# Kernel tuning notes

Measured on AMD Instinct MI355X. Metric: run time of the kernel, lower is better.

Reference implementation:

```python
import jax, jax.numpy as jnp
import numpy as np

B, N, N_IN, N_HID, N_OUT, T = 64, 64, 64, 256, 64, 4
E = N * (N - 1)  # 4032 directed edges, fully connected minus self-loops


def _incidence():
    # off-diagonal sender/receiver index pairs, NRI-style one-hot matrices
    send_idx, rec_idx = [], []
    for i in range(N):
        for j in range(N):
            if i != j:
                send_idx.append(i)
                rec_idx.append(j)
    eye = np.eye(N, dtype=np.float32)
    rel_send = eye[np.array(send_idx)]  # [E, N]
    rel_rec = eye[np.array(rec_idx)]    # [E, N]
    return jnp.asarray(rel_rec), jnp.asarray(rel_send)


def setup_inputs() -> dict:
    key = jax.random.key(0)
    ks = jax.random.split(key, 16)
    rel_rec, rel_send = _incidence()
    s1 = 1.0 / np.sqrt(2 * N_IN)
    s2 = 1.0 / np.sqrt(N_HID)
    s3 = 1.0 / np.sqrt(N_IN + N_OUT)
    return {
        "x": jax.random.normal(ks[0], (B, N, N_IN), jnp.float32),
        "rel_type": jax.random.uniform(ks[1], (B, E, T), jnp.float32),
        "rel_rec": rel_rec,
        "rel_send": rel_send,
        # per-edge-type message MLPs, stored as [T, in, out] (torch Linear transposed)
        "w1": jax.random.uniform(ks[2], (T, 2 * N_IN, N_HID), jnp.float32, -s1, s1),
        "b1": jax.random.uniform(ks[3], (T, N_HID), jnp.float32, -s1, s1),
        "w2": jax.random.uniform(ks[4], (T, N_HID, N_OUT), jnp.float32, -s2, s2),
        "b2": jax.random.uniform(ks[5], (T, N_OUT), jnp.float32, -s2, s2),
        "ow1": jax.random.uniform(ks[6], (N_IN + N_OUT, N_HID), jnp.float32, -s3, s3),
        "ob1": jax.random.uniform(ks[7], (N_HID,), jnp.float32, -s3, s3),
        "ow2": jax.random.uniform(ks[8], (N_HID, N_HID), jnp.float32, -s2, s2),
        "ob2": jax.random.uniform(ks[9], (N_HID,), jnp.float32, -s2, s2),
        "ow3": jax.random.uniform(ks[10], (N_HID, N_OUT), jnp.float32, -s2, s2),
        "ob3": jax.random.uniform(ks[11], (N_OUT,), jnp.float32, -s2, s2),
    }


def reference(x, rel_type, rel_rec, rel_send, w1, b1, w2, b2, ow1, ob1, ow2, ob2, ow3, ob3):
    # node2edge gather: [E,N] @ [B,N,F] -> [B,E,F]
    receivers = jnp.einsum('en,bnf->bef', rel_rec, x)
    senders = jnp.einsum('en,bnf->bef', rel_send, x)
    pre_msg = jnp.concatenate([senders, receivers], axis=-1)  # [B,E,2F]
    all_msgs = jnp.zeros((pre_msg.shape[0], pre_msg.shape[1], w2.shape[-1]), pre_msg.dtype)
    for i in range(w1.shape[0]):  # small fixed edge_types loop (structurally distinct weights)
        m = jax.nn.relu(pre_msg @ w1[i] + b1[i])           # [B,E,H]
        m = jax.nn.relu(m @ w2[i] + b2[i])                 # [B,E,O]
        all_msgs = all_msgs + m * rel_type[:, :, i:i + 1]  # weighted accumulate
    # edge2node scatter-aggregate: [N,E] @ [B,E,O] -> [B,N,O]
    agg_msgs = jnp.einsum('en,beo->bno', rel_rec, all_msgs)
    aug = jnp.concatenate([x, agg_msgs], axis=-1)          # [B,N,F+O]
    h = jax.nn.relu(aug @ ow1 + ob1)
    h = jax.nn.relu(h @ ow2 + ob2)
    return h @ ow3 + ob3                                   # [B,N,O]
```

## Files before the change

kernel.cpp:

```cpp
#include <hip/hip_runtime.h>

typedef unsigned short u16;
typedef __attribute__((ext_vector_type(8))) _Float16 f16x8;
typedef __attribute__((ext_vector_type(2))) _Float16 f16x2;
typedef __attribute__((ext_vector_type(4))) float f32x4;

#define DEV static __device__ __forceinline__

DEV float bf2f(u16 h){ unsigned u = ((unsigned)h) << 16; return __builtin_bit_cast(float, u); }
DEV u16 f2bf(float f){ unsigned u = __builtin_bit_cast(unsigned, f); u += 0x7FFFu + ((u >> 16) & 1u); return (u16)(u >> 16); }
DEV u16 f2h(float f){ _Float16 h = (_Float16)f; return __builtin_bit_cast(u16, h); }
DEV float h2f(u16 h){ return (float)__builtin_bit_cast(_Float16, h); }

DEV f32x4 mfma16(f16x8 a, f16x8 b, f32x4 c){
  return __builtin_amdgcn_mfma_f32_16x16x32_f16(a, b, c, 0, 0, 0);
}

DEV unsigned rap(unsigned a, unsigned b){
  f16x2 ha = __builtin_bit_cast(f16x2, a);
  f16x2 hb = __builtin_bit_cast(f16x2, b);
  f16x2 s = ha + hb;
  const _Float16 z = (_Float16)0;
  s.x = s.x > z ? s.x : z;
  s.y = s.y > z ? s.y : z;
  return __builtin_bit_cast(unsigned, s);
}

DEV f16x8 build_frag(uint4 s, uint4 r){
  uint4 o;
  o.x = rap(s.x, r.x); o.y = rap(s.y, r.y);
  o.z = rap(s.z, r.z); o.w = rap(s.w, r.w);
  return __builtin_bit_cast(f16x8, o);
}

#define OFF_W1T  256
#define OFF_W2T  262400
#define OFF_OW1T 393472
#define OFF_OW2T 459008
#define OFF_OW3T 590080
#define OFF_B1   622848
#define OFF_B2   624896
#define OFF_OB1  625408
#define OFF_OB2  625920
#define OFF_OB3  626432
#define OFF_XC   626688
#define OFF_RTC  1150976
#define OFF_S1   3215360
#define OFF_R1   11603968
#define OFF_AGG  19992576

__global__ void k_sniff(const u16* __restrict__ x, int* __restrict__ flag){
  int l = threadIdx.x;
  u16 u = x[2 * l];
  int e = (u >> 7) & 0xFF;
  int ok = (e >= 103 && e <= 143) ? 1 : 0;
  unsigned long long m = __ballot(ok);
  if(l == 0) *flag = (__builtin_popcountll(m) >= 40) ? 1 : 0;
}

DEV float ldin(const void* p, int i, int isbf){
  return isbf ? bf2f(((const u16*)p)[i]) : ((const float*)p)[i];
}

__global__ __launch_bounds__(256) void k_tr(const void* __restrict__ w1, const void* __restrict__ w2,
    const void* __restrict__ ow1, const void* __restrict__ ow2, const void* __restrict__ ow3,
    char* __restrict__ ws){
  const int isbf = *(const int*)ws;
  __shared__ float tile[32][33];
  int bid = blockIdx.x, tid = threadIdx.x;
  const void* src; u16* dst; int R, C, off, r0, c0;
  if(bid < 128){ int g = bid >> 5, tt = bid & 31;
    src = w1; dst = (u16*)(ws + OFF_W1T); R = 128; C = 256; off = g * 32768;
    r0 = (tt >> 3) << 5; c0 = (tt & 7) << 5;
  } else if(bid < 192){ int bb = bid - 128; int g = bb >> 4, tt = bb & 15;
    src = w2; dst = (u16*)(ws + OFF_W2T); R = 256; C = 64; off = g * 16384;
    r0 = (tt >> 1) << 5; c0 = (tt & 1) << 5;
  } else if(bid < 224){ int bb = bid - 192;
    src = ow1; dst = (u16*)(ws + OFF_OW1T); R = 128; C = 256; off = 0;
    r0 = (bb >> 3) << 5; c0 = (bb & 7) << 5;
  } else if(bid < 288){ int bb = bid - 224;
    src = ow2; dst = (u16*)(ws + OFF_OW2T); R = 256; C = 256; off = 0;
    r0 = (bb >> 3) << 5; c0 = (bb & 7) << 5;
  } else { int bb = bid - 288;
    src = ow3; dst = (u16*)(ws + OFF_OW3T); R = 256; C = 64; off = 0;
    r0 = (bb >> 1) << 5; c0 = (bb & 1) << 5;
  }
  int tx = tid & 31, ty = tid >> 5;
  #pragma unroll
  for(int p = 0; p < 4; ++p){
    int r = ty + p * 8;
    tile[r][tx] = ldin(src, off + (r0 + r) * C + c0 + tx, isbf);
  }
  __syncthreads();
  #pragma unroll
  for(int p = 0; p < 4; ++p){
    int c = ty + p * 8;
    dst[off + (c0 + c) * R + r0 + tx] = f2h(tile[tx][c]);
  }
}

__global__ __launch_bounds__(256) void k_cvt2(const void* __restrict__ x, const void* __restrict__ rt,
    const void* __restrict__ b1, const void* __restrict__ b2,
    const void* __restrict__ ob1, const void* __restrict__ ob2, const void* __restrict__ ob3,
    char* __restrict__ ws){
  const int isbf = *(const int*)ws;
  int n = blockIdx.x * 256 + threadIdx.x;
  if(n < 262144){ ((u16*)(ws+OFF_XC))[n] = f2h(ldin(x, n, isbf)); return; }
  n -= 262144;
  if(n < 1032192){ ((u16*)(ws+OFF_RTC))[n] = f2h(ldin(rt, n, isbf)); return; }
  n -= 1032192;
  if(n < 1024){ ((u16*)(ws+OFF_B1))[n] = f2h(ldin(b1, n, isbf)); return; }
  n -= 1024;
  if(n < 256){ ((u16*)(ws+OFF_B2))[n] = f2h(ldin(b2, n, isbf)); return; }
  n -= 256;
  if(n < 256){ ((u16*)(ws+OFF_OB1))[n] = f2h(ldin(ob1, n, isbf)); return; }
  n -= 256;
  if(n < 256){ ((u16*)(ws+OFF_OB2))[n] = f2h(ldin(ob2, n, isbf)); return; }
  n -= 256;
  if(n < 64){ ((u16*)(ws+OFF_OB3))[n] = f2h(ldin(ob3, n, isbf)); return; }
}

__global__ __launch_bounds__(256) void k_s1r1(const u16* __restrict__ Xc, const u16* __restrict__ W1T,
    const u16* __restrict__ B1c, u16* __restrict__ S1, u16* __restrict__ R1){
  __shared__ __align__(16) u16 sX[64][72];
  __shared__ __align__(16) u16 sW[256][72];
  const int tid = threadIdx.x, bid = blockIdx.x;
  const int b = bid & 63, th = bid >> 6, t = th >> 1, half = th & 1;
  {
    const uint4* src = (const uint4*)(Xc + b*4096);
    #pragma unroll
    for(int it=0; it<2; ++it){
      int c = tid + it*256; int row = c >> 3, col = (c & 7) * 8;
      *(uint4*)&sX[row][col] = src[c];
    }
    const u16* base = W1T + t*32768 + half*64;
    #pragma unroll
    for(int it=0; it<8; ++it){
      int c = tid + it*256; int h = c >> 3, kc = (c & 7) * 8;
      *(uint4*)&sW[h][kc] = *(const uint4*)(base + h*128 + kc);
    }
  }
  __syncthreads();
  const int wv = tid >> 6, l = tid & 63, ml = l & 15, q = l >> 4;
  const f32x4 z = {0.f,0.f,0.f,0.f};
  f32x4 acc[4][4];
  #pragma unroll
  for(int mt=0;mt<4;++mt){ acc[mt][0]=z; acc[mt][1]=z; acc[mt][2]=z; acc[mt][3]=z; }
  #pragma unroll
  for(int ks=0; ks<2; ++ks){
    const int kb = ks*32 + q*8;
    f16x8 af[4], bff[4];
    #pragma unroll
    for(int mt=0;mt<4;++mt) af[mt] = *(const f16x8*)&sX[mt*16 + ml][kb];
    #pragma unroll
    for(int nt=0;nt<4;++nt) bff[nt] = *(const f16x8*)&sW[wv*64 + nt*16 + ml][kb];
    #pragma unroll
    for(int mt=0;mt<4;++mt)
      #pragma unroll
      for(int nt=0;nt<4;++nt)
        acc[mt][nt] = mfma16(af[mt], bff[nt], acc[mt][nt]);
  }
  u16* dst = (half ? R1 : S1) + (t*64 + b)*16384;
  #pragma unroll
  for(int nt=0;nt<4;++nt){
    const int h = wv*64 + nt*16 + ml;
    const float bias = half ? h2f(B1c[t*256 + h]) : 0.0f;
    #pragma unroll
    for(int mt=0;mt<4;++mt)
      #pragma unroll
      for(int r=0;r<4;++r){
        int irow = mt*16 + q*4 + r;
        dst[irow*256 + h] = f2h(acc[mt][nt][r] + bias);
      }
  }
}

__global__ __launch_bounds__(256, 1) void k_edge(const u16* __restrict__ RTc, const u16* __restrict__ W2T,
    const u16* __restrict__ B2c, const u16* __restrict__ S1, const u16* __restrict__ R1,
    float* __restrict__ AGG){
  __shared__ float sRTa[4][16][64];
  __shared__ float sAggB[1024];
  const int tid = threadIdx.x;
  const int t = tid >> 6, l = tid & 63, ml = l & 15, q = l >> 4;
  const int b = blockIdx.x >> 2, j0 = (blockIdx.x & 3) * 16;
  #pragma unroll
  for(int it=0; it<4; ++it) sAggB[it*256 + tid] = 0.0f;
  #pragma unroll 1
  for(int jj=0; jj<16; ++jj){
    int j = j0 + jj, i = l;
    float v = 0.0f;
    if(i != j){ int e = i*63 + j - (j > i ? 1 : 0); v = h2f(RTc[(b*4032 + e)*4 + t]); }
    sRTa[t][jj][i] = v;
  }
  __syncthreads();
  f16x8 bfr[4][8];
  {
    const u16* w2t = W2T + t*16384;
    #pragma unroll
    for(int nt=0;nt<4;++nt)
      #pragma unroll
      for(int ks=0;ks<8;++ks)
        bfr[nt][ks] = *(const f16x8*)(w2t + (nt*16 + ml)*256 + ks*32 + q*8);
  }
  uint4 su[4][8];
  const u16* s1b = S1 + (t*64 + b)*16384;
  #pragma unroll
  for(int mt=0;mt<4;++mt)
    #pragma unroll
    for(int ks=0;ks<8;++ks)
      su[mt][ks] = *(const uint4*)(s1b + (mt*16 + ml)*256 + ks*32 + q*8);
  float bias2[4];
  #pragma unroll
  for(int nt=0;nt<4;++nt) bias2[nt] = h2f(B2c[t*64 + nt*16 + ml]);
  const u16* r1b = R1 + (t*64 + b)*16384;
  const f32x4 z = {0.f,0.f,0.f,0.f};
  uint4 ru[8], run[8];
  #pragma unroll
  for(int ks=0;ks<8;++ks) ru[ks] = *(const uint4*)(r1b + j0*256 + ks*32 + q*8);
  #pragma unroll 1
  for(int jj=0; jj<16; ++jj){
    if(jj < 15){
      const u16* r1n = r1b + (j0 + jj + 1)*256;
      #pragma unroll
      for(int ks=0;ks<8;++ks) run[ks] = *(const uint4*)(r1n + ks*32 + q*8);
    }
    f32x4 acc[4][4];
    #pragma unroll
    for(int mt=0;mt<4;++mt){ acc[mt][0]=z; acc[mt][1]=z; acc[mt][2]=z; acc[mt][3]=z; }
    #pragma unroll
    for(int ks=0;ks<8;++ks){
      #pragma unroll
      for(int mt=0;mt<4;++mt){
        f16x8 af = build_frag(su[mt][ks], ru[ks]);
        #pragma unroll
        for(int nt=0;nt<4;++nt) acc[mt][nt] = mfma16(af, bfr[nt][ks], acc[mt][nt]);
      }
    }
    float cs[4] = {0.f,0.f,0.f,0.f};
    #pragma unroll
    for(int mt=0;mt<4;++mt){
      float rw[4];
      #pragma unroll
      for(int r=0;r<4;++r) rw[r] = sRTa[t][jj][mt*16 + q*4 + r];
      #pragma unroll
      for(int nt=0;nt<4;++nt)
        #pragma unroll
        for(int r=0;r<4;++r)
          cs[nt] += fmaxf(acc[mt][nt][r] + bias2[nt], 0.0f) * rw[r];
    }
    #pragma unroll
    for(int nt=0;nt<4;++nt){
      float v = cs[nt];
      v += __shfl_xor(v, 16, 64);
      v += __shfl_xor(v, 32, 64);
      if(q == 0) atomicAdd(&sAggB[jj*64 + nt*16 + ml], v);
    }
    #pragma unroll
    for(int ks=0;ks<8;++ks) ru[ks] = run[ks];
  }
  __syncthreads();
  float* aggb = AGG + (b*64 + j0)*64;
  #pragma unroll
  for(int it=0; it<4; ++it) aggb[it*256 + tid] = sAggB[it*256 + tid];
}

__global__ __launch_bounds__(256) void k_node(const u16* __restrict__ Xc, const float* __restrict__ AGG,
    const u16* __restrict__ OW1T, const u16* __restrict__ OB1c,
    const u16* __restrict__ OW2T, const u16* __restrict__ OB2c,
    const u16* __restrict__ OW3T, const u16* __restrict__ OB3c,
    void* __restrict__ out, const int* __restrict__ flag){
  __shared__ __align__(16) u16 sA[64][136];
  __shared__ __align__(16) u16 sH[64][264];
  __shared__ __align__(16) u16 sH2[64][264];
  __shared__ __align__(16) u16 sW[64][264];
  const int tid = threadIdx.x, bb = blockIdx.x;
  const int isbf = *flag;
  {
    const uint4* src = (const uint4*)(Xc + bb*4096);
    #pragma unroll
    for(int it=0; it<2; ++it){
      int c = tid + it*256; int row = c >> 3, col = (c & 7)*8;
      *(uint4*)&sA[row][col] = src[c];
    }
    const float* ag = AGG + bb*4096;
    #pragma unroll
    for(int it=0; it<16; ++it){
      int c = tid + it*256; int row = c >> 6, col = c & 63;
      sA[row][64 + col] = f2h(ag[c]);
    }
  }
  const int wv = tid >> 6, l = tid & 63, ml = l & 15, q = l >> 4;
  const f32x4 z = {0.f,0.f,0.f,0.f};
  __syncthreads();
  for(int nc=0; nc<4; ++nc){
    #pragma unroll
    for(int it=0; it<4; ++it){
      int c = tid + it*256; int h = c >> 4, kc = (c & 15)*8;
      *(uint4*)&sW[h][kc] = *(const uint4*)(OW1T + (nc*64 + h)*128 + kc);
    }
    __syncthreads();
    f32x4 acc[4] = {z,z,z,z};
    #pragma unroll
    for(int ks=0; ks<4; ++ks){
      int kb = ks*32 + q*8;
      f16x8 bfrag = *(const f16x8*)&sW[wv*16 + ml][kb];
      #pragma unroll
      for(int mt=0;mt<4;++mt){
        f16x8 afrag = *(const f16x8*)&sA[mt*16 + ml][kb];
        acc[mt] = mfma16(afrag, bfrag, acc[mt]);
      }
    }
    const int h = nc*64 + wv*16 + ml;
    const float bias = h2f(OB1c[h]);
    #pragma unroll
    for(int mt=0;mt<4;++mt)
      #pragma unroll
      for(int r=0;r<4;++r){
        int row = mt*16 + q*4 + r;
        sH[row][h] = f2h(fmaxf(acc[mt][r] + bias, 0.0f));
      }
    __syncthreads();
  }
  for(int nc=0; nc<4; ++nc){
    #pragma unroll
    for(int it=0; it<8; ++it){
      int c = tid + it*256; int h = c >> 5, kc = (c & 31)*8;
      *(uint4*)&sW[h][kc] = *(const uint4*)(OW2T + (nc*64 + h)*256 + kc);
    }
    __syncthreads();
    f32x4 acc[4] = {z,z,z,z};
    #pragma unroll
    for(int ks=0; ks<8; ++ks){
      int kb = ks*32 + q*8;
      f16x8 bfrag = *(const f16x8*)&sW[wv*16 + ml][kb];
      #pragma unroll
      for(int mt=0;mt<4;++mt){
        f16x8 afrag = *(const f16x8*)&sH[mt*16 + ml][kb];
        acc[mt] = mfma16(afrag, bfrag, acc[mt]);
      }
    }
    const int h = nc*64 + wv*16 + ml;
    const float bias = h2f(OB2c[h]);
    #pragma unroll
    for(int mt=0;mt<4;++mt)
      #pragma unroll
      for(int r=0;r<4;++r){
        int row = mt*16 + q*4 + r;
        sH2[row][h] = f2h(fmaxf(acc[mt][r] + bias, 0.0f));
      }
    __syncthreads();
  }
  {
    #pragma unroll
    for(int it=0; it<8; ++it){
      int c = tid + it*256; int h = c >> 5, kc = (c & 31)*8;
      *(uint4*)&sW[h][kc] = *(const uint4*)(OW3T + h*256 + kc);
    }
    __syncthreads();
    f32x4 acc[4] = {z,z,z,z};
    #pragma unroll
    for(int ks=0; ks<8; ++ks){
      int kb = ks*32 + q*8;
      f16x8 bfrag = *(const f16x8*)&sW[wv*16 + ml][kb];
      #pragma unroll
      for(int mt=0;mt<4;++mt){
        f16x8 afrag = *(const f16x8*)&sH2[mt*16 + ml][kb];
        acc[mt] = mfma16(afrag, bfrag, acc[mt]);
      }
    }
    const int o = wv*16 + ml;
    const float bias = h2f(OB3c[o]);
    #pragma unroll
    for(int mt=0;mt<4;++mt)
      #pragma unroll
      for(int r=0;r<4;++r){
        int row = mt*16 + q*4 + r;
        float v = acc[mt][r] + bias;
        int idx = bb*4096 + row*64 + o;
        if(isbf) ((u16*)out)[idx] = f2bf(v);
        else     ((float*)out)[idx] = v;
      }
  }
}

extern "C" void kernel_launch(void* const* d_in, const int* in_sizes, int n_in,
                              void* d_out, int out_size, void* d_ws, size_t ws_size,
                              hipStream_t stream){
  (void)in_sizes; (void)n_in; (void)out_size; (void)ws_size;
  char* ws = (char*)d_ws;
  u16* W1T  = (u16*)(ws + OFF_W1T);
  u16* W2T  = (u16*)(ws + OFF_W2T);
  u16* OW1T = (u16*)(ws + OFF_OW1T);
  u16* OW2T = (u16*)(ws + OFF_OW2T);
  u16* OW3T = (u16*)(ws + OFF_OW3T);
  u16* B1c  = (u16*)(ws + OFF_B1);
  u16* B2c  = (u16*)(ws + OFF_B2);
  u16* OB1c = (u16*)(ws + OFF_OB1);
  u16* OB2c = (u16*)(ws + OFF_OB2);
  u16* OB3c = (u16*)(ws + OFF_OB3);
  u16* Xc   = (u16*)(ws + OFF_XC);
  u16* RTc  = (u16*)(ws + OFF_RTC);
  u16* S1   = (u16*)(ws + OFF_S1);
  u16* R1   = (u16*)(ws + OFF_R1);
  float* AGG = (float*)(ws + OFF_AGG);

  k_sniff<<<1, 64, 0, stream>>>((const u16*)d_in[0], (int*)ws);
  k_tr<<<304, 256, 0, stream>>>(d_in[4], d_in[6], d_in[8], d_in[10], d_in[12], ws);
  k_cvt2<<<5064, 256, 0, stream>>>(d_in[0], d_in[1], d_in[5], d_in[7],
                                   d_in[9], d_in[11], d_in[13], ws);
  k_s1r1<<<512, 256, 0, stream>>>(Xc, W1T, B1c, S1, R1);
  k_edge<<<256, 256, 0, stream>>>(RTc, W2T, B2c, S1, R1, AGG);
  k_node<<<64, 256, 0, stream>>>(Xc, AGG, OW1T, OB1c, OW2T, OB2c, OW3T, OB3c, d_out, (const int*)ws);
}
```

Before: 170.7 us.

## Fuse prep kernels, convert inputs inline, restructure edge kernel per edge type

Merges the sniff, transpose and bias-convert kernels into one prep launch, and drops the standalone conversion of x and rel_type by converting them inside the consumers. The edge kernel now splits work by edge type across blocks. It stages S1 and W2 in shared memory, processes two receivers per wave for more MFMA reuse, and writes per-type partial aggregates in fp16 instead of using shared-memory atomics. The node kernel sums the four partials. This removes launches and a large conversion pass, at the cost of extra partial-aggregate traffic and lower fp16 accumulation precision.

```diff
diff --git a/kernel.cpp b/kernel.cpp
--- a/kernel.cpp
+++ b/kernel.cpp
@@ -43,31 +43,51 @@
 #define OFF_OB1  625408
 #define OFF_OB2  625920
 #define OFF_OB3  626432
-#define OFF_XC   626688
-#define OFF_RTC  1150976
-#define OFF_S1   3215360
-#define OFF_R1   11603968
-#define OFF_AGG  19992576
-
-__global__ void k_sniff(const u16* __restrict__ x, int* __restrict__ flag){
-  int l = threadIdx.x;
-  u16 u = x[2 * l];
-  int e = (u >> 7) & 0xFF;
-  int ok = (e >= 103 && e <= 143) ? 1 : 0;
-  unsigned long long m = __ballot(ok);
-  if(l == 0) *flag = (__builtin_popcountll(m) >= 40) ? 1 : 0;
-}
+#define OFF_S1   626688
+#define OFF_R1   9015296
+#define OFF_AGGT 17403904
 
 DEV float ldin(const void* p, int i, int isbf){
   return isbf ? bf2f(((const u16*)p)[i]) : ((const float*)p)[i];
 }
 
-__global__ __launch_bounds__(256) void k_tr(const void* __restrict__ w1, const void* __restrict__ w2,
-    const void* __restrict__ ow1, const void* __restrict__ ow2, const void* __restrict__ ow3,
+DEV int sniff_isbf(const u16* x, int tid, int* sflag){
+  if(tid < 64){
+    u16 u = x[2 * tid];
+    int e = (u >> 7) & 0xFF;
+    int ok = (e >= 103 && e <= 143) ? 1 : 0;
+    unsigned long long m = __ballot(ok);
+    if(tid == 0) *sflag = (__builtin_popcountll(m) >= 40) ? 1 : 0;
+  }
+  __syncthreads();
+  return *sflag;
+}
+
+__global__ __launch_bounds__(256) void k_prep(const void* __restrict__ x,
+    const void* __restrict__ w1, const void* __restrict__ b1,
+    const void* __restrict__ w2, const void* __restrict__ b2,
+    const void* __restrict__ ow1, const void* __restrict__ ob1,
+    const void* __restrict__ ow2, const void* __restrict__ ob2,
+    const void* __restrict__ ow3, const void* __restrict__ ob3,
     char* __restrict__ ws){
-  const int isbf = *(const int*)ws;
   __shared__ float tile[32][33];
-  int bid = blockIdx.x, tid = threadIdx.x;
+  __shared__ int sflag;
+  const int bid = blockIdx.x, tid = threadIdx.x;
+  const int isbf = sniff_isbf((const u16*)x, tid, &sflag);
+  if(bid == 312){ if(tid == 0) *(int*)ws = isbf; return; }
+  if(bid >= 304){
+    int n = (bid - 304) * 256 + tid;
+    if(n < 1024){ ((u16*)(ws+OFF_B1))[n] = f2h(ldin(b1, n, isbf)); return; }
+    n -= 1024;
+    if(n < 256){ ((u16*)(ws+OFF_B2))[n] = f2h(ldin(b2, n, isbf)); return; }
+    n -= 256;
+    if(n < 256){ ((u16*)(ws+OFF_OB1))[n] = f2h(ldin(ob1, n, isbf)); return; }
+    n -= 256;
+    if(n < 256){ ((u16*)(ws+OFF_OB2))[n] = f2h(ldin(ob2, n, isbf)); return; }
+    n -= 256;
+    if(n < 64){ ((u16*)(ws+OFF_OB3))[n] = f2h(ldin(ob3, n, isbf)); }
+    return;
+  }
   const void* src; u16* dst; int R, C, off, r0, c0;
   if(bid < 128){ int g = bid >> 5, tt = bid & 31;
     src = w1; dst = (u16*)(ws + OFF_W1T); R = 128; C = 256; off = g * 32768;
@@ -99,39 +119,37 @@
   }
 }
 
-__global__ __launch_bounds__(256) void k_cvt2(const void* __restrict__ x, const void* __restrict__ rt,
-    const void* __restrict__ b1, const void* __restrict__ b2,
-    const void* __restrict__ ob1, const void* __restrict__ ob2, const void* __restrict__ ob3,
-    char* __restrict__ ws){
-  const int isbf = *(const int*)ws;
-  int n = blockIdx.x * 256 + threadIdx.x;
-  if(n < 262144){ ((u16*)(ws+OFF_XC))[n] = f2h(ldin(x, n, isbf)); return; }
-  n -= 262144;
-  if(n < 1032192){ ((u16*)(ws+OFF_RTC))[n] = f2h(ldin(rt, n, isbf)); return; }
-  n -= 1032192;
-  if(n < 1024){ ((u16*)(ws+OFF_B1))[n] = f2h(ldin(b1, n, isbf)); return; }
-  n -= 1024;
-  if(n < 256){ ((u16*)(ws+OFF_B2))[n] = f2h(ldin(b2, n, isbf)); return; }
-  n -= 256;
-  if(n < 256){ ((u16*)(ws+OFF_OB1))[n] = f2h(ldin(ob1, n, isbf)); return; }
-  n -= 256;
-  if(n < 256){ ((u16*)(ws+OFF_OB2))[n] = f2h(ldin(ob2, n, isbf)); return; }
-  n -= 256;
-  if(n < 64){ ((u16*)(ws+OFF_OB3))[n] = f2h(ldin(ob3, n, isbf)); return; }
-}
-
-__global__ __launch_bounds__(256) void k_s1r1(const u16* __restrict__ Xc, const u16* __restrict__ W1T,
-    const u16* __restrict__ B1c, u16* __restrict__ S1, u16* __restrict__ R1){
+__global__ __launch_bounds__(256) void k_s1r1(const void* __restrict__ x, const u16* __restrict__ W1T,
+    const u16* __restrict__ B1c, u16* __restrict__ S1, u16* __restrict__ R1,
+    const int* __restrict__ flag){
   __shared__ __align__(16) u16 sX[64][72];
   __shared__ __align__(16) u16 sW[256][72];
   const int tid = threadIdx.x, bid = blockIdx.x;
   const int b = bid & 63, th = bid >> 6, t = th >> 1, half = th & 1;
+  const int isbf = *flag;
   {
-    const uint4* src = (const uint4*)(Xc + b*4096);
-    #pragma unroll
-    for(int it=0; it<2; ++it){
-      int c = tid + it*256; int row = c >> 3, col = (c & 7) * 8;
-      *(uint4*)&sX[row][col] = src[c];
+    if(isbf){
+      const uint4* src = (const uint4*)((const u16*)x + b*4096);
+      #pragma unroll
+      for(int it=0; it<2; ++it){
+        int c = tid + it*256; int row = c >> 3, col = (c & 7) * 8;
+        uint4 v = src[c];
+        const u16* pv = (const u16*)&v;
+        u16 o[8];
+        #pragma unroll
+        for(int e=0;e<8;++e) o[e] = f2h(bf2f(pv[e]));
+        *(uint4*)&sX[row][col] = *(const uint4*)o;
+      }
+    } else {
+      const float* src = (const float*)x + b*4096;
+      #pragma unroll
+      for(int it=0; it<2; ++it){
+        int c = tid + it*256; int row = c >> 3, col = (c & 7) * 8;
+        u16 o[8];
+        #pragma unroll
+        for(int e=0;e<8;++e) o[e] = f2h(src[c*8 + e]);
+        *(uint4*)&sX[row][col] = *(const uint4*)o;
+      }
     }
     const u16* base = W1T + t*32768 + half*64;
     #pragma unroll
@@ -175,96 +193,111 @@
   }
 }
 
-__global__ __launch_bounds__(256, 1) void k_edge(const u16* __restrict__ RTc, const u16* __restrict__ W2T,
-    const u16* __restrict__ B2c, const u16* __restrict__ S1, const u16* __restrict__ R1,
-    float* __restrict__ AGG){
-  __shared__ float sRTa[4][16][64];
-  __shared__ float sAggB[1024];
-  const int tid = threadIdx.x;
-  const int t = tid >> 6, l = tid & 63, ml = l & 15, q = l >> 4;
-  const int b = blockIdx.x >> 2, j0 = (blockIdx.x & 3) * 16;
-  #pragma unroll
-  for(int it=0; it<4; ++it) sAggB[it*256 + tid] = 0.0f;
-  #pragma unroll 1
-  for(int jj=0; jj<16; ++jj){
-    int j = j0 + jj, i = l;
-    float v = 0.0f;
-    if(i != j){ int e = i*63 + j - (j > i ? 1 : 0); v = h2f(RTc[(b*4032 + e)*4 + t]); }
-    sRTa[t][jj][i] = v;
+#define EPI(ACC, JL) { \
+  float cs0=0.f, cs1=0.f, cs2=0.f, cs3=0.f; \
+  _Pragma("unroll") \
+  for(int mt=0;mt<4;++mt){ \
+    f32x4 rw = *(const f32x4*)&sRT[JL][mt*16 + q*4]; \
+    _Pragma("unroll") \
+    for(int r=0;r<4;++r){ \
+      cs0 += fmaxf(ACC[mt][0][r] + bias2[0], 0.0f) * rw[r]; \
+      cs1 += fmaxf(ACC[mt][1][r] + bias2[1], 0.0f) * rw[r]; \
+      cs2 += fmaxf(ACC[mt][2][r] + bias2[2], 0.0f) * rw[r]; \
+      cs3 += fmaxf(ACC[mt][3][r] + bias2[3], 0.0f) * rw[r]; \
+    } \
+  } \
+  float csa[4] = {cs0, cs1, cs2, cs3}; \
+  u16* dstp = AGGT + (((t*64 + b)*64) + (j0 + (JL)))*64; \
+  _Pragma("unroll") \
+  for(int nt=0;nt<4;++nt){ \
+    float v = csa[nt]; \
+    v += __shfl_xor(v, 16, 64); \
+    v += __shfl_xor(v, 32, 64); \
+    if(q == 0) dstp[nt*16 + ml] = f2h(v); \
+  } \
+}
+
+__global__ __launch_bounds__(256, 2) void k_edge(const void* __restrict__ rt,
+    const u16* __restrict__ W2T, const u16* __restrict__ B2c,
+    const u16* __restrict__ S1, const u16* __restrict__ R1,
+    u16* __restrict__ AGGT, const int* __restrict__ flag){
+  __shared__ __align__(16) u16 sS1[64][264];
+  __shared__ __align__(16) u16 sW2[64][264];
+  __shared__ float sRT[32][64];
+  const int tid = threadIdx.x, bid = blockIdx.x;
+  const int t = bid >> 7, b = (bid >> 1) & 63, jg = bid & 1, j0 = jg * 32;
+  const int isbf = *flag;
+  {
+    const uint4* s1p = (const uint4*)(S1 + (t*64 + b)*16384);
+    const uint4* w2p = (const uint4*)(W2T + t*16384);
+    #pragma unroll
+    for(int it=0; it<8; ++it){
+      int c = tid + it*256;
+      int row = c >> 5, col = (c & 31) * 8;
+      *(uint4*)&sS1[row][col] = s1p[c];
+      *(uint4*)&sW2[row][col] = w2p[c];
+    }
+    #pragma unroll
+    for(int it=0; it<8; ++it){
+      int c = tid + it*256;
+      int jl = c >> 6, i = c & 63, j = j0 + jl;
+      float v = 0.0f;
+      if(i != j){
+        int e = i*63 + j - (j > i ? 1 : 0);
+        v = ldin(rt, (b*4032 + e)*4 + t, isbf);
+      }
+      sRT[jl][i] = v;
+    }
   }
   __syncthreads();
-  f16x8 bfr[4][8];
-  {
-    const u16* w2t = W2T + t*16384;
-    #pragma unroll
-    for(int nt=0;nt<4;++nt)
-      #pragma unroll
-      for(int ks=0;ks<8;++ks)
-        bfr[nt][ks] = *(const f16x8*)(w2t + (nt*16 + ml)*256 + ks*32 + q*8);
-  }
-  uint4 su[4][8];
-  const u16* s1b = S1 + (t*64 + b)*16384;
-  #pragma unroll
-  for(int mt=0;mt<4;++mt)
-    #pragma unroll
-    for(int ks=0;ks<8;++ks)
-      su[mt][ks] = *(const uint4*)(s1b + (mt*16 + ml)*256 + ks*32 + q*8);
+  const int w = tid >> 6, l = tid & 63, ml = l & 15, q = l >> 4;
   float bias2[4];
   #pragma unroll
   for(int nt=0;nt<4;++nt) bias2[nt] = h2f(B2c[t*64 + nt*16 + ml]);
   const u16* r1b = R1 + (t*64 + b)*16384;
   const f32x4 z = {0.f,0.f,0.f,0.f};
-  uint4 ru[8], run[8];
-  #pragma unroll
-  for(int ks=0;ks<8;++ks) ru[ks] = *(const uint4*)(r1b + j0*256 + ks*32 + q*8);
   #pragma unroll 1
-  for(int jj=0; jj<16; ++jj){
-    if(jj < 15){
-      const u16* r1n = r1b + (j0 + jj + 1)*256;
-      #pragma unroll
-      for(int ks=0;ks<8;++ks) run[ks] = *(const uint4*)(r1n + ks*32 + q*8);
-    }
-    f32x4 acc[4][4];
-    #pragma unroll
-    for(int mt=0;mt<4;++mt){ acc[mt][0]=z; acc[mt][1]=z; acc[mt][2]=z; acc[mt][3]=z; }
+  for(int jp=0; jp<4; ++jp){
+    const int jA = w*8 + jp*2, jB = jA + 1;
+    uint4 ruA[8], ruB[8];
+    {
+      const u16* rA = r1b + (j0 + jA)*256;
+      const u16* rB = r1b + (j0 + jB)*256;
+      #pragma unroll
+      for(int ks=0;ks<8;++ks){
+        ruA[ks] = *(const uint4*)(rA + ks*32 + q*8);
+        ruB[ks] = *(const uint4*)(rB + ks*32 + q*8);
+      }
+    }
+    f32x4 accA[4][4], accB[4][4];
+    #pragma unroll
+    for(int mt=0;mt<4;++mt)
+      #pragma unroll
+      for(int nt=0;nt<4;++nt){ accA[mt][nt]=z; accB[mt][nt]=z; }
     #pragma unroll
     for(int ks=0;ks<8;++ks){
+      const int kb = ks*32 + q*8;
+      f16x8 bf[4];
+      #pragma unroll
+      for(int nt=0;nt<4;++nt) bf[nt] = *(const f16x8*)&sW2[nt*16 + ml][kb];
       #pragma unroll
       for(int mt=0;mt<4;++mt){
-        f16x8 af = build_frag(su[mt][ks], ru[ks]);
+        uint4 su = *(const uint4*)&sS1[mt*16 + ml][kb];
+        f16x8 afA = build_frag(su, ruA[ks]);
+        f16x8 afB = build_frag(su, ruB[ks]);
         #pragma unroll
-        for(int nt=0;nt<4;++nt) acc[mt][nt] = mfma16(af, bfr[nt][ks], acc[mt][nt]);
-      }
-    }
-    float cs[4] = {0.f,0.f,0.f,0.f};
-    #pragma unroll
-    for(int mt=0;mt<4;++mt){
-      float rw[4];
-      #pragma unroll
-      for(int r=0;r<4;++r) rw[r] = sRTa[t][jj][mt*16 + q*4 + r];
-      #pragma unroll
-      for(int nt=0;nt<4;++nt)
-        #pragma unroll
-        for(int r=0;r<4;++r)
-          cs[nt] += fmaxf(acc[mt][nt][r] + bias2[nt], 0.0f) * rw[r];
-    }
-    #pragma unroll
-    for(int nt=0;nt<4;++nt){
-      float v = cs[nt];
-      v += __shfl_xor(v, 16, 64);
-      v += __shfl_xor(v, 32, 64);
-      if(q == 0) atomicAdd(&sAggB[jj*64 + nt*16 + ml], v);
-    }
-    #pragma unroll
-    for(int ks=0;ks<8;++ks) ru[ks] = run[ks];
-  }
-  __syncthreads();
-  float* aggb = AGG + (b*64 + j0)*64;
-  #pragma unroll
-  for(int it=0; it<4; ++it) aggb[it*256 + tid] = sAggB[it*256 + tid];
-}
-
-__global__ __launch_bounds__(256) void k_node(const u16* __restrict__ Xc, const float* __restrict__ AGG,
+        for(int nt=0;nt<4;++nt){
+          accA[mt][nt] = mfma16(afA, bf[nt], accA[mt][nt]);
+          accB[mt][nt] = mfma16(afB, bf[nt], accB[mt][nt]);
+        }
+      }
+    }
+    EPI(accA, jA)
+    EPI(accB, jB)
+  }
+}
+
+__global__ __launch_bounds__(256) void k_node(const void* __restrict__ x, const u16* __restrict__ AGGT,
     const u16* __restrict__ OW1T, const u16* __restrict__ OB1c,
     const u16* __restrict__ OW2T, const u16* __restrict__ OB2c,
     const u16* __restrict__ OW3T, const u16* __restrict__ OB3c,
@@ -276,17 +309,37 @@
   const int tid = threadIdx.x, bb = blockIdx.x;
   const int isbf = *flag;
   {
-    const uint4* src = (const uint4*)(Xc + bb*4096);
-    #pragma unroll
-    for(int it=0; it<2; ++it){
-      int c = tid + it*256; int row = c >> 3, col = (c & 7)*8;
-      *(uint4*)&sA[row][col] = src[c];
-    }
-    const float* ag = AGG + bb*4096;
+    if(isbf){
+      const uint4* src = (const uint4*)((const u16*)x + bb*4096);
+      #pragma unroll
+      for(int it=0; it<2; ++it){
+        int c = tid + it*256; int row = c >> 3, col = (c & 7)*8;
+        uint4 v = src[c];
+        const u16* pv = (const u16*)&v;
+        u16 o[8];
+        #pragma unroll
+        for(int e=0;e<8;++e) o[e] = f2h(bf2f(pv[e]));
+        *(uint4*)&sA[row][col] = *(const uint4*)o;
+      }
+    } else {
+      const float* src = (const float*)x + bb*4096;
+      #pragma unroll
+      for(int it=0; it<2; ++it){
+        int c = tid + it*256; int row = c >> 3, col = (c & 7)*8;
+        u16 o[8];
+        #pragma unroll
+        for(int e=0;e<8;++e) o[e] = f2h(src[c*8 + e]);
+        *(uint4*)&sA[row][col] = *(const uint4*)o;
+      }
+    }
     #pragma unroll
     for(int it=0; it<16; ++it){
       int c = tid + it*256; int row = c >> 6, col = c & 63;
-      sA[row][64 + col] = f2h(ag[c]);
+      float s = 0.0f;
+      #pragma unroll
+      for(int tt=0; tt<4; ++tt)
+        s += h2f(AGGT[(((tt*64 + bb)*64) + row)*64 + col]);
+      sA[row][64 + col] = f2h(s);
     }
   }
   const int wv = tid >> 6, l = tid & 63, ml = l & 15, q = l >> 4;
@@ -398,17 +451,14 @@
   u16* OB1c = (u16*)(ws + OFF_OB1);
   u16* OB2c = (u16*)(ws + OFF_OB2);
   u16* OB3c = (u16*)(ws + OFF_OB3);
-  u16* Xc   = (u16*)(ws + OFF_XC);
-  u16* RTc  = (u16*)(ws + OFF_RTC);
   u16* S1   = (u16*)(ws + OFF_S1);
   u16* R1   = (u16*)(ws + OFF_R1);
-  float* AGG = (float*)(ws + OFF_AGG);
-
-  k_sniff<<<1, 64, 0, stream>>>((const u16*)d_in[0], (int*)ws);
-  k_tr<<<304, 256, 0, stream>>>(d_in[4], d_in[6], d_in[8], d_in[10], d_in[12], ws);
-  k_cvt2<<<5064, 256, 0, stream>>>(d_in[0], d_in[1], d_in[5], d_in[7],
-                                   d_in[9], d_in[11], d_in[13], ws);
-  k_s1r1<<<512, 256, 0, stream>>>(Xc, W1T, B1c, S1, R1);
-  k_edge<<<256, 256, 0, stream>>>(RTc, W2T, B2c, S1, R1, AGG);
-  k_node<<<64, 256, 0, stream>>>(Xc, AGG, OW1T, OB1c, OW2T, OB2c, OW3T, OB3c, d_out, (const int*)ws);
-}
+  u16* AGGT = (u16*)(ws + OFF_AGGT);
+  const int* flag = (const int*)ws;
+
+  k_prep<<<313, 256, 0, stream>>>(d_in[0], d_in[4], d_in[5], d_in[6], d_in[7],
+                                  d_in[8], d_in[9], d_in[10], d_in[11], d_in[12], d_in[13], ws);
+  k_s1r1<<<512, 256, 0, stream>>>(d_in[0], W1T, B1c, S1, R1, flag);
+  k_edge<<<512, 256, 0, stream>>>(d_in[1], W2T, B2c, S1, R1, AGGT, flag);
+  k_node<<<64, 256, 0, stream>>>(d_in[0], AGGT, OW1T, OB1c, OW2T, OB2c, OW3T, OB3c, d_out, flag);
+}
```

After: 209.1 us. 1.22x slower.
